# Kernel tuning notes

Hardware: AMD Instinct MI355X
Metric: run time of the kernel (lower is better)

Reference implementation:

```python
import jax, jax.numpy as jnp
import numpy as np

N = 100000   # nodes
E = 1250000  # edges
R = 8        # num_relations
D = 64       # in_channels = hidden = out dim (all 64 per RGIN_Net construction)
L = 2        # max_depth
EPS = 1e-5


def setup_inputs() -> dict:
    key = jax.random.key(0)
    ks = jax.random.split(key, 18)
    s = 1.0 / np.sqrt(D)
    inp = {
        'x': jax.random.normal(ks[0], (N, D), dtype=jnp.float32),
        'edge_index': jax.random.randint(ks[1], (2, E), 0, N, dtype=jnp.int64),
        'edge_type': jax.random.randint(ks[2], (E,), 0, R, dtype=jnp.int64),
        # per-relation MLP params, stacked over L layers and R relations
        'W1': jax.random.normal(ks[3], (L, R, D, D), dtype=jnp.float32) * s,
        'b1': jax.random.normal(ks[4], (L, R, D), dtype=jnp.float32) * 0.01,
        'g1': 1.0 + 0.1 * jax.random.normal(ks[5], (L, R, D), dtype=jnp.float32),
        'be1': jax.random.normal(ks[6], (L, R, D), dtype=jnp.float32) * 0.01,
        'W2': jax.random.normal(ks[7], (L, R, D, D), dtype=jnp.float32) * s,
        'b2': jax.random.normal(ks[8], (L, R, D), dtype=jnp.float32) * 0.01,
        # root MLP params per layer
        'rW1': jax.random.normal(ks[9], (L, D, D), dtype=jnp.float32) * s,
        'rb1': jax.random.normal(ks[10], (L, D), dtype=jnp.float32) * 0.01,
        'rg1': 1.0 + 0.1 * jax.random.normal(ks[11], (L, D), dtype=jnp.float32),
        'rbe1': jax.random.normal(ks[12], (L, D), dtype=jnp.float32) * 0.01,
        'rW2': jax.random.normal(ks[13], (L, D, D), dtype=jnp.float32) * s,
        'rb2': jax.random.normal(ks[14], (L, D), dtype=jnp.float32) * 0.01,
        'bias': jax.random.normal(ks[15], (L, D), dtype=jnp.float32) * 0.01,
    }
    return inp


def _bn(z, gamma, beta, axis):
    # BatchNorm1d in training mode: batch stats, biased variance
    mean = jnp.mean(z, axis=axis, keepdims=True)
    var = jnp.mean(jnp.square(z - mean), axis=axis, keepdims=True)
    return (z - mean) * jax.lax.rsqrt(var + EPS) * gamma + beta


def _forward(x, edge_index, edge_type, W1, b1, g1, be1, W2, b2,
             rW1, rb1, rg1, rbe1, rW2, rb2, bias):
    src, dst = edge_index[0], edge_index[1]
    # combined segment id encodes (relation, dst-node) -> one fused scatter-add
    seg = edge_type * N + dst
    for i in range(L):
        # gather -> scatter-add per relation: h[r, n] = sum_{e: type=r, dst=n} x[src[e]]
        h = jax.ops.segment_sum(x[src], seg, num_segments=R * N).reshape(R, N, D)
        # per-relation MLP: Linear -> BN -> ReLU -> Linear (summed over relations)
        z = jnp.einsum('rnd,rdh->rnh', h, W1[i]) + b1[i][:, None, :]
        z = jax.nn.relu(_bn(z, g1[i][:, None, :], be1[i][:, None, :], axis=1))
        rel = jnp.einsum('rnh,rho->rno', z, W2[i]) + b2[i][:, None, :]
        out = rel.sum(axis=0)
        # root MLP on x itself
        zr = x @ rW1[i] + rb1[i]
        zr = jax.nn.relu(_bn(zr, rg1[i], rbe1[i], axis=0))
        out = out + zr @ rW2[i] + rb2[i] + bias[i]
        x = jax.nn.relu(out) if i + 1 < L else out  # dropout p=0.0
    return x


def reference(x, edge_index, edge_type, W1, b1, g1, be1, W2, b2,
              rW1, rb1, rg1, rbe1, rW2, rb2, bias):
    return _forward(x, edge_index, edge_type, W1, b1, g1, be1, W2, b2,
                    rW1, rb1, rg1, rbe1, rW2, rb2, bias)
```

## Files before the change

### kernel.cpp

```cpp
#include <hip/hip_runtime.h>

#define NN 100000
#define NE 1250000
#define NR 8
#define DD 64
#define TILE 128
#define NTILES 782
#define NBUCKETS (NR * NTILES)
#define CAP 512
#define HROW 72
#define EPSB 1e-5f

typedef unsigned short u16;
typedef unsigned int u32;
typedef __attribute__((ext_vector_type(8))) short short8;
typedef __attribute__((ext_vector_type(4))) float f32x4;

static __device__ __forceinline__ float b2f_lo(u32 v) { return __uint_as_float(v << 16); }
static __device__ __forceinline__ float b2f_hi(u32 v) { return __uint_as_float(v & 0xffff0000u); }
static __device__ __forceinline__ u16 f2b(float f) {
    u32 u = __float_as_uint(f);
    u += 0x7fffu + ((u >> 16) & 1u);
    return (u16)(u >> 16);
}
static __device__ __forceinline__ u32 pk(float a, float b) {
    return (u32)f2b(a) | ((u32)f2b(b) << 16);
}
static __device__ __forceinline__ void acc8(float* acc, uint4 v0, uint4 v1, uint4 v2, uint4 v3) {
#pragma unroll
    for (int q = 0; q < 4; q++) {
        uint4 v = (q == 0) ? v0 : (q == 1) ? v1 : (q == 2) ? v2 : v3;
        acc[q * 8 + 0] += b2f_lo(v.x);
        acc[q * 8 + 1] += b2f_hi(v.x);
        acc[q * 8 + 2] += b2f_lo(v.y);
        acc[q * 8 + 3] += b2f_hi(v.y);
        acc[q * 8 + 4] += b2f_lo(v.z);
        acc[q * 8 + 5] += b2f_hi(v.z);
        acc[q * 8 + 6] += b2f_lo(v.w);
        acc[q * 8 + 7] += b2f_hi(v.w);
    }
}


__global__ void cvt_kernel(const float* __restrict__ in, u16* __restrict__ outb) {
    int i = blockIdx.x * 256 + threadIdx.x;
    if (i < NN * DD / 8) {
        float4 a = *(const float4*)&in[i * 8];
        float4 b = *(const float4*)&in[i * 8 + 4];
        uint4 o;
        o.x = pk(a.x, a.y); o.y = pk(a.z, a.w);
        o.z = pk(b.x, b.y); o.w = pk(b.z, b.w);
        *(uint4*)&outb[i * 8] = o;
    }
}


__global__ void wt_kernel(const float* __restrict__ W1, const float* __restrict__ rW1,
                          const float* __restrict__ W2, const float* __restrict__ rW2,
                          u16* __restrict__ wt1g, u16* __restrict__ wt2g) {
    int m = blockIdx.x;
    int i = m / 18, rest = m % 18;
    int set = rest / 9, r = rest % 9;
    const float* W = (set == 0)
        ? ((r < NR) ? (W1 + ((size_t)i * NR + r) * DD * DD) : (rW1 + (size_t)i * DD * DD))
        : ((r < NR) ? (W2 + ((size_t)i * NR + r) * DD * DD) : (rW2 + (size_t)i * DD * DD));
    u32* dst = (u32*)((set == 0 ? wt1g : wt2g) + ((size_t)i * 9 + r) * DD * DD);
    for (int j = threadIdx.x; j < DD * 32; j += 256) {
        int d = j >> 5, kp = j & 31;
        dst[j] = pk(W[(2 * kp) * DD + d], W[(2 * kp + 1) * DD + d]);
    }
}


__global__ void count_kernel(const int* __restrict__ dst,
                             const int* __restrict__ et,
                             int* __restrict__ cnt) {
    int i = blockIdx.x * 256 + threadIdx.x;
    if (i < NE) atomicAdd(&cnt[et[i] * NTILES + (dst[i] >> 7)], 1);
}

__global__ void scan_kernel(const int* __restrict__ cnt, int* __restrict__ off, int n) {
    __shared__ int ts[1024];
    int t = threadIdx.x;
    int v[8];
    int s = 0;
#pragma unroll
    for (int j = 0; j < 8; j++) {
        int idx = t * 8 + j;
        int c = (idx < n) ? cnt[idx] : 0;
        v[j] = s;
        s += c;
    }
    ts[t] = s;
    __syncthreads();
    for (int d = 1; d < 1024; d <<= 1) {
        int add = (t >= d) ? ts[t - d] : 0;
        __syncthreads();
        ts[t] += add;
        __syncthreads();
    }
    int base = (t > 0) ? ts[t - 1] : 0;
#pragma unroll
    for (int j = 0; j < 8; j++) {
        int idx = t * 8 + j;
        if (idx < n) off[idx] = base + v[j];
    }
    if (t == 1023) off[n] = ts[1023];
}

__global__ void fill_kernel(const int* __restrict__ src, const int* __restrict__ dst,
                            const int* __restrict__ et, const int* __restrict__ off,
                            int* __restrict__ cursor, int* __restrict__ ep) {
    int i = blockIdx.x * 256 + threadIdx.x;
    if (i < NE) {
        int d = dst[i];
        int b = et[i] * NTILES + (d >> 7);
        int pos = off[b] + atomicAdd(&cursor[b], 1);
        ep[pos] = (src[i] << 8) | (d & 127);
    }
}


__launch_bounds__(256, 4)
__global__ void gemm1_kernel(const u16* __restrict__ xb,
                             const int* __restrict__ ep, const int* __restrict__ off,
                             const u16* __restrict__ wt1, const float* __restrict__ b1l,
                             const float* __restrict__ rb1l,
                             u16* __restrict__ zb, float* __restrict__ stats) {
    __shared__ u16 hsb[TILE * HROW];
    __shared__ int seS[CAP], seD[CAP];
    __shared__ int shist[TILE], scur[TILE], soff[TILE + 1];
    __shared__ float red[2 * DD];
    int r = blockIdx.y;
    bool root = (r == NR);
    int n0 = blockIdx.x * TILE;
    int tid = threadIdx.x;

    int wv = tid >> 6;
    int l  = tid & 63;
    int lr = l & 15;
    int lg = l >> 4;

    const u16* wtg = wt1 + (size_t)r * DD * DD;
    short8 bfrg[2][4];
#pragma unroll
    for (int ks = 0; ks < 2; ks++)
#pragma unroll
        for (int ct = 0; ct < 4; ct++)
            bfrg[ks][ct] = *(const short8*)&wtg[(ct * 16 + lr) * DD + ks * 32 + lg * 8];

    if (tid < 128) red[tid] = 0.f;

    if (!root) {
        int b = r * NTILES + blockIdx.x;
        int e0 = off[b], e1 = off[b + 1];
        int m = e1 - e0;
        int slot = tid & 127, half = tid >> 7;
        float acc[32];
#pragma unroll
        for (int j = 0; j < 32; j++) acc[j] = 0.f;

        for (int base = 0; base < m; base += CAP) {
            int cnt = min(m - base, CAP);
            if (tid < TILE) shist[tid] = 0;
            __syncthreads();
            for (int i = tid; i < cnt; i += 256) {
                int p = ep[e0 + base + i];
                seS[i] = p;
                atomicAdd(&shist[p & 127], 1);
            }
            __syncthreads();
            if (tid < TILE) soff[tid + 1] = shist[tid];
            if (tid == 0) soff[0] = 0;
            __syncthreads();
            for (int d = 1; d < TILE; d <<= 1) {
                int v = 0;
                if (tid < TILE && tid >= d) v = soff[tid + 1 - d];
                __syncthreads();
                if (tid < TILE && tid >= d) soff[tid + 1] += v;
                __syncthreads();
            }
            if (tid < TILE) scur[tid] = soff[tid];
            __syncthreads();
            for (int i = tid; i < cnt; i += 256) {
                int p = seS[i];
                seD[atomicAdd(&scur[p & 127], 1)] = p;
            }
            __syncthreads();
            int sb = soff[slot], se = soff[slot + 1];
            int e = sb;
            for (; e + 2 <= se; e += 2) {
                const u16* xr0 = &xb[(size_t)(seD[e] >> 8) * DD + half * 32];
                const u16* xr1 = &xb[(size_t)(seD[e + 1] >> 8) * DD + half * 32];
                uint4 a0 = *(const uint4*)(xr0);      uint4 c0 = *(const uint4*)(xr1);
                uint4 a1 = *(const uint4*)(xr0 + 8);  uint4 c1 = *(const uint4*)(xr1 + 8);
                uint4 a2 = *(const uint4*)(xr0 + 16); uint4 c2 = *(const uint4*)(xr1 + 16);
                uint4 a3 = *(const uint4*)(xr0 + 24); uint4 c3 = *(const uint4*)(xr1 + 24);
                acc8(acc, a0, a1, a2, a3);
                acc8(acc, c0, c1, c2, c3);
            }
            if (e < se) {
                const u16* xr = &xb[(size_t)(seD[e] >> 8) * DD + half * 32];
                acc8(acc, *(const uint4*)(xr), *(const uint4*)(xr + 8),
                     *(const uint4*)(xr + 16), *(const uint4*)(xr + 24));
            }
            __syncthreads();
        }
        u32 pw[16];
#pragma unroll
        for (int j = 0; j < 16; j++) pw[j] = pk(acc[2 * j], acc[2 * j + 1]);
        u16* hrow = &hsb[slot * HROW + half * 32];
        *(uint4*)(hrow)      = make_uint4(pw[0], pw[1], pw[2], pw[3]);
        *(uint4*)(hrow + 8)  = make_uint4(pw[4], pw[5], pw[6], pw[7]);
        *(uint4*)(hrow + 16) = make_uint4(pw[8], pw[9], pw[10], pw[11]);
        *(uint4*)(hrow + 24) = make_uint4(pw[12], pw[13], pw[14], pw[15]);
    } else {
        for (int idx = tid; idx < TILE * 8; idx += 256) {
            int row = idx >> 3, q = idx & 7;
            int n = n0 + row;
            uint4 v = make_uint4(0, 0, 0, 0);
            if (n < NN) v = *(const uint4*)&xb[(size_t)n * DD + q * 8];
            *(uint4*)&hsb[row * HROW + q * 8] = v;
        }
    }
    __syncthreads();

    f32x4 dacc[2][4];
#pragma unroll
    for (int rt = 0; rt < 2; rt++)
#pragma unroll
        for (int ct = 0; ct < 4; ct++) dacc[rt][ct] = (f32x4){0.f, 0.f, 0.f, 0.f};

#pragma unroll
    for (int ks = 0; ks < 2; ks++) {
        short8 afr[2];
#pragma unroll
        for (int rt = 0; rt < 2; rt++)
            afr[rt] = *(const short8*)&hsb[(wv * 32 + rt * 16 + lr) * HROW + ks * 32 + lg * 8];
#pragma unroll
        for (int ct = 0; ct < 4; ct++) {
            dacc[0][ct] = __builtin_amdgcn_mfma_f32_16x16x32_bf16(afr[0], bfrg[ks][ct], dacc[0][ct], 0, 0, 0);
            dacc[1][ct] = __builtin_amdgcn_mfma_f32_16x16x32_bf16(afr[1], bfrg[ks][ct], dacc[1][ct], 0, 0, 0);
        }
    }

    const float* bvec = root ? rb1l : (b1l + r * DD);
    float bv4[4], s1v[4], s2v[4];
#pragma unroll
    for (int ct = 0; ct < 4; ct++) { bv4[ct] = bvec[16 * ct + lr]; s1v[ct] = 0.f; s2v[ct] = 0.f; }
#pragma unroll
    for (int rt = 0; rt < 2; rt++)
#pragma unroll
        for (int ct = 0; ct < 4; ct++)
#pragma unroll
            for (int i = 0; i < 4; i++) {
                float v = dacc[rt][ct][i] + bv4[ct];
                dacc[rt][ct][i] = v;
                int n = n0 + wv * 32 + rt * 16 + lg * 4 + i;
                if (n < NN) { s1v[ct] += v; s2v[ct] += v * v; }
            }
#pragma unroll
    for (int ct = 0; ct < 4; ct++) {
        float a = s1v[ct], bq = s2v[ct];
        a += __shfl_xor(a, 16); bq += __shfl_xor(bq, 16);
        a += __shfl_xor(a, 32); bq += __shfl_xor(bq, 32);
        if (lg == 0) {
            atomicAdd(&red[16 * ct + lr], a);
            atomicAdd(&red[64 + 16 * ct + lr], bq);
        }
    }
    __syncthreads();

#pragma unroll
    for (int rt = 0; rt < 2; rt++)
#pragma unroll
        for (int ct = 0; ct < 4; ct++)
#pragma unroll
            for (int i = 0; i < 4; i++)
                hsb[(wv * 32 + rt * 16 + lg * 4 + i) * HROW + 16 * ct + lr] = f2b(dacc[rt][ct][i]);
    __syncthreads();

    u16* zout = zb + (size_t)r * NN * DD;
    for (int idx = tid; idx < TILE * 8; idx += 256) {
        int row = idx >> 3, q = idx & 7;
        int n = n0 + row;
        if (n < NN)
            *(uint4*)&zout[(size_t)n * DD + q * 8] = *(const uint4*)&hsb[row * HROW + q * 8];
    }
    if (tid < 64) {
        atomicAdd(&stats[r * DD + tid], red[tid]);
        atomicAdd(&stats[576 + r * DD + tid], red[64 + tid]);
    }
}


__global__ void finalize_kernel(const float* __restrict__ stats,
                                const float* __restrict__ g1l, const float* __restrict__ be1l,
                                const float* __restrict__ rg1l, const float* __restrict__ rbe1l,
                                const float* __restrict__ b2l, const float* __restrict__ rb2l,
                                const float* __restrict__ biasl,
                                float* __restrict__ affine, float* __restrict__ constd) {
    int t = threadIdx.x;
    if (t < 576) {
        int r = t >> 6, d = t & 63;
        float mean = stats[t] * (1.f / NN);
        float var = fmaxf(stats[576 + t] * (1.f / NN) - mean * mean, 0.f);
        float g  = (r < NR) ? g1l[r * DD + d]  : rg1l[d];
        float be = (r < NR) ? be1l[r * DD + d] : rbe1l[d];
        float sc = g * rsqrtf(var + EPSB);
        affine[t] = sc;
        affine[576 + t] = be - mean * sc;
        if (r == 0) {
            float cd = rb2l[d] + biasl[d];
#pragma unroll
            for (int rr = 0; rr < NR; rr++) cd += b2l[rr * DD + d];
            constd[d] = cd;
        }
    }
}


__launch_bounds__(256, 4)
__global__ void pass2_kernel(const u16* __restrict__ zb, const u16* __restrict__ wt2,
                             const float* __restrict__ affine, const float* __restrict__ constd,
                             float* __restrict__ outf, u16* __restrict__ outb,
                             int emit_bf16_relu) {
    __shared__ u16 zsb[TILE * HROW];
    __shared__ u16 wtb[DD * HROW];
    int n0 = blockIdx.x * TILE;
    int tid = threadIdx.x;
    int srow = tid >> 3;
    int sc0 = (tid & 7) * 8;

    int wv = tid >> 6;
    int l  = tid & 63;
    int lr = l & 15;
    int lg = l >> 4;

    f32x4 dacc[2][4];
#pragma unroll
    for (int rt = 0; rt < 2; rt++)
#pragma unroll
        for (int ct = 0; ct < 4; ct++) dacc[rt][ct] = (f32x4){0.f, 0.f, 0.f, 0.f};

    uint4 preA[4], preB[4];
#pragma unroll
    for (int q = 0; q < 4; q++) {
        int n = n0 + srow + 32 * q;
        preA[q] = (n < NN) ? *(const uint4*)&zb[(size_t)n * DD + sc0] : make_uint4(0, 0, 0, 0);
        preB[q] = (n < NN) ? *(const uint4*)&zb[(size_t)NN * DD + (size_t)n * DD + sc0]
                           : make_uint4(0, 0, 0, 0);
    }

#pragma unroll
    for (int r = 0; r < 9; r++) {
        uint4* cur = (r & 1) ? preB : preA;
        float4 aLo = *(const float4*)&affine[r * DD + sc0];
        float4 aHi = *(const float4*)&affine[r * DD + sc0 + 4];
        float4 cLo = *(const float4*)&affine[576 + r * DD + sc0];
        float4 cHi = *(const float4*)&affine[576 + r * DD + sc0 + 4];
        __syncthreads();
#pragma unroll
        for (int q = 0; q < 4; q++) {
            uint4 vv = cur[q];
            float a0 = fmaxf(fmaf(b2f_lo(vv.x), aLo.x, cLo.x), 0.f);
            float a1 = fmaxf(fmaf(b2f_hi(vv.x), aLo.y, cLo.y), 0.f);
            float a2 = fmaxf(fmaf(b2f_lo(vv.y), aLo.z, cLo.z), 0.f);
            float a3 = fmaxf(fmaf(b2f_hi(vv.y), aLo.w, cLo.w), 0.f);
            float a4 = fmaxf(fmaf(b2f_lo(vv.z), aHi.x, cHi.x), 0.f);
            float a5 = fmaxf(fmaf(b2f_hi(vv.z), aHi.y, cHi.y), 0.f);
            float a6 = fmaxf(fmaf(b2f_lo(vv.w), aHi.z, cHi.z), 0.f);
            float a7 = fmaxf(fmaf(b2f_hi(vv.w), aHi.w, cHi.w), 0.f);
            uint4 o = make_uint4(pk(a0, a1), pk(a2, a3), pk(a4, a5), pk(a6, a7));
            *(uint4*)&zsb[(srow + 32 * q) * HROW + sc0] = o;
        }
        {
            const u32* wsrc = (const u32*)(wt2 + (size_t)r * DD * DD);
            for (int i2 = tid; i2 < DD * 32; i2 += 256) {
                int row = i2 >> 5, q = i2 & 31;
                ((u32*)&wtb[row * HROW])[q] = wsrc[i2];
            }
        }
        __syncthreads();
        if (r + 2 < 9) {
            const u16* zp = zb + (size_t)(r + 2) * NN * DD;
#pragma unroll
            for (int q = 0; q < 4; q++) {
                int n = n0 + srow + 32 * q;
                cur[q] = (n < NN) ? *(const uint4*)&zp[(size_t)n * DD + sc0]
                                  : make_uint4(0, 0, 0, 0);
            }
        }
#pragma unroll
        for (int ks = 0; ks < 2; ks++) {
            short8 afr[2];
#pragma unroll
            for (int rt = 0; rt < 2; rt++)
                afr[rt] = *(const short8*)&zsb[(wv * 32 + rt * 16 + lr) * HROW + ks * 32 + lg * 8];
#pragma unroll
            for (int ct = 0; ct < 4; ct++) {
                short8 bfr = *(const short8*)&wtb[(ct * 16 + lr) * HROW + ks * 32 + lg * 8];
                dacc[0][ct] = __builtin_amdgcn_mfma_f32_16x16x32_bf16(afr[0], bfr, dacc[0][ct], 0, 0, 0);
                dacc[1][ct] = __builtin_amdgcn_mfma_f32_16x16x32_bf16(afr[1], bfr, dacc[1][ct], 0, 0, 0);
            }
        }
    }

    float cd4[4];
#pragma unroll
    for (int ct = 0; ct < 4; ct++) cd4[ct] = constd[16 * ct + lr];

    if (emit_bf16_relu) {
        __syncthreads();
#pragma unroll
        for (int rt = 0; rt < 2; rt++)
#pragma unroll
            for (int ct = 0; ct < 4; ct++)
#pragma unroll
                for (int i = 0; i < 4; i++) {
                    float v = fmaxf(dacc[rt][ct][i] + cd4[ct], 0.f);
                    zsb[(wv * 32 + rt * 16 + lg * 4 + i) * HROW + 16 * ct + lr] = f2b(v);
                }
        __syncthreads();
        for (int idx = tid; idx < TILE * 8; idx += 256) {
            int row = idx >> 3, q = idx & 7;
            int n = n0 + row;
            if (n < NN)
                *(uint4*)&outb[(size_t)n * DD + q * 8] = *(const uint4*)&zsb[row * HROW + q * 8];
        }
    } else {
        float* zf = (float*)zsb;
#pragma unroll
        for (int h = 0; h < 2; h++) {
            __syncthreads();
#pragma unroll
            for (int rt = 0; rt < 2; rt++)
#pragma unroll
                for (int cc = 0; cc < 2; cc++) {
                    int ct = 2 * h + cc;
#pragma unroll
                    for (int i = 0; i < 4; i++)
                        zf[(wv * 32 + rt * 16 + lg * 4 + i) * 34 + 16 * cc + lr] =
                            dacc[rt][ct][i] + cd4[ct];
                }
            __syncthreads();
            for (int idx = tid; idx < TILE * 8; idx += 256) {
                int row = idx >> 3, q = idx & 7;
                int n = n0 + row;
                if (n < NN)
                    *(float4*)&outf[(size_t)n * DD + 32 * h + q * 4] =
                        *(const float4*)&zf[row * 34 + q * 4];
            }
        }
    }
}


extern "C" void kernel_launch(void* const* d_in, const int* in_sizes, int n_in,
                              void* d_out, int out_size, void* d_ws, size_t ws_size,
                              hipStream_t stream) {
    (void)in_sizes; (void)n_in; (void)out_size;

    const float* x0   = (const float*)d_in[0];
    const int*   ei   = (const int*)d_in[1];
    const int*   et   = (const int*)d_in[2];
    const float* W1   = (const float*)d_in[3];
    const float* b1   = (const float*)d_in[4];
    const float* g1   = (const float*)d_in[5];
    const float* be1  = (const float*)d_in[6];
    const float* W2   = (const float*)d_in[7];
    const float* b2   = (const float*)d_in[8];
    const float* rW1  = (const float*)d_in[9];
    const float* rb1  = (const float*)d_in[10];
    const float* rg1  = (const float*)d_in[11];
    const float* rbe1 = (const float*)d_in[12];
    const float* rW2  = (const float*)d_in[13];
    const float* rb2  = (const float*)d_in[14];
    const float* bias = (const float*)d_in[15];
    float* out = (float*)d_out;

    char* ws = (char*)d_ws;
    size_t zelems = (size_t)9 * NN * DD;
    u16* zb   = (u16*)ws;
    u16* xb   = zb + zelems;
    u16* wt1g = xb + (size_t)NN * DD;
    u16* wt2g = wt1g + 18 * DD * DD;
    float* stats  = (float*)(wt2g + 18 * DD * DD);
    float* affine = stats + 1152;
    float* constd = affine + 1152;
    int* cnt    = (int*)(constd + 64);
    int* cursor = cnt + NBUCKETS;
    int* off    = cursor + NBUCKETS;
    int* ep     = off + NBUCKETS + 1;

    size_t need = (zelems + (size_t)NN * DD + 36 * DD * DD) * 2
                + (1152 + 1152 + 64) * 4
                + ((size_t)3 * NBUCKETS + 1 + NE) * 4;
    if (ws_size < need) return;

    cvt_kernel<<<(NN * DD / 8 + 255) / 256, 256, 0, stream>>>(x0, xb);
    wt_kernel<<<36, 256, 0, stream>>>(W1, rW1, W2, rW2, wt1g, wt2g);
    hipMemsetAsync(cnt, 0, sizeof(int) * 2 * NBUCKETS, stream);
    count_kernel<<<(NE + 255) / 256, 256, 0, stream>>>(ei + NE, et, cnt);
    scan_kernel<<<1, 1024, 0, stream>>>(cnt, off, NBUCKETS);
    fill_kernel<<<(NE + 255) / 256, 256, 0, stream>>>(ei, ei + NE, et, off, cursor, ep);

    for (int i = 0; i < 2; i++) {
        hipMemsetAsync(stats, 0, sizeof(float) * 1152, stream);
        gemm1_kernel<<<dim3(NTILES, 9), 256, 0, stream>>>(
            xb, ep, off,
            wt1g + (size_t)i * 9 * DD * DD,
            b1 + (size_t)i * NR * DD, rb1 + (size_t)i * DD,
            zb, stats);
        finalize_kernel<<<1, 576, 0, stream>>>(
            stats,
            g1 + (size_t)i * NR * DD, be1 + (size_t)i * NR * DD,
            rg1 + (size_t)i * DD, rbe1 + (size_t)i * DD,
            b2 + (size_t)i * NR * DD, rb2 + (size_t)i * DD, bias + (size_t)i * DD,
            affine, constd);
        pass2_kernel<<<NTILES, 256, 0, stream>>>(
            zb, wt2g + (size_t)i * 9 * DD * DD,
            affine, constd, out, xb, (i == 0) ? 1 : 0);
    }
}
```

Measured before the change: 493.7 us.

## Use wave-shuffle bucket scan, prefetch W2 into registers, raise gemm1 occupancy

In gemm1, the barrier-heavy shared-memory prefix scan over the 128 per-tile histogram bins becomes a single-wave shuffle scan, and the trailing barrier of the chunk loop is dropped. The weight-fragment load moves after the gather phase so its registers are not live during accumulation, and launch bounds go from 4 to 6 blocks per CU. In gemm2, the next relation's W2 tile is prefetched into registers during the current MFMA phase rather than loaded synchronously into LDS. Raising the occupancy target risks register spills in the gather loop.

Measured after the change: 500.8 us. About the same (+1.4%).

```diff
diff --git a/kernel.cpp b/kernel.cpp
--- a/kernel.cpp
+++ b/kernel.cpp
@@ -121,7 +121,7 @@
 }
 
 
-__launch_bounds__(256, 4)
+__launch_bounds__(256, 6)
 __global__ void gemm1_kernel(const u16* __restrict__ xb,
                              const int* __restrict__ ep, const int* __restrict__ off,
                              const u16* __restrict__ wt1, const float* __restrict__ b1l,
@@ -129,7 +129,8 @@
                              u16* __restrict__ zb, float* __restrict__ stats) {
     __shared__ u16 hsb[TILE * HROW];
     __shared__ int seS[CAP], seD[CAP];
-    __shared__ int shist[TILE], scur[TILE], soff[TILE + 1];
+    __shared__ int shist[TILE], scur[TILE];
+    __shared__ int soff[TILE + 1];
     __shared__ float red[2 * DD];
     int r = blockIdx.y;
     bool root = (r == NR);
@@ -140,14 +141,6 @@
     int l  = tid & 63;
     int lr = l & 15;
     int lg = l >> 4;
-
-    const u16* wtg = wt1 + (size_t)r * DD * DD;
-    short8 bfrg[2][4];
-#pragma unroll
-    for (int ks = 0; ks < 2; ks++)
-#pragma unroll
-        for (int ct = 0; ct < 4; ct++)
-            bfrg[ks][ct] = *(const short8*)&wtg[(ct * 16 + lr) * DD + ks * 32 + lg * 8];
 
     if (tid < 128) red[tid] = 0.f;
 
@@ -170,17 +163,22 @@
                 atomicAdd(&shist[p & 127], 1);
             }
             __syncthreads();
-            if (tid < TILE) soff[tid + 1] = shist[tid];
-            if (tid == 0) soff[0] = 0;
-            __syncthreads();
-            for (int d = 1; d < TILE; d <<= 1) {
-                int v = 0;
-                if (tid < TILE && tid >= d) v = soff[tid + 1 - d];
-                __syncthreads();
-                if (tid < TILE && tid >= d) soff[tid + 1] += v;
-                __syncthreads();
-            }
-            if (tid < TILE) scur[tid] = soff[tid];
+            if (tid < 64) {
+                int c0 = shist[tid], c1 = shist[tid + 64];
+                int s0 = c0, s1 = c1;
+#pragma unroll
+                for (int d = 1; d < 64; d <<= 1) {
+                    int t0 = __shfl_up(s0, d);
+                    int t1 = __shfl_up(s1, d);
+                    if (tid >= d) { s0 += t0; s1 += t1; }
+                }
+                int tot0 = __shfl(s0, 63);
+                soff[tid + 1]  = s0;
+                soff[tid + 65] = tot0 + s1;
+                if (tid == 0) soff[0] = 0;
+                scur[tid]      = s0 - c0;
+                scur[tid + 64] = tot0 + s1 - c1;
+            }
             __syncthreads();
             for (int i = tid; i < cnt; i += 256) {
                 int p = seS[i];
@@ -204,7 +202,6 @@
                 acc8(acc, *(const uint4*)(xr), *(const uint4*)(xr + 8),
                      *(const uint4*)(xr + 16), *(const uint4*)(xr + 24));
             }
-            __syncthreads();
         }
         u32 pw[16];
 #pragma unroll
@@ -223,6 +220,14 @@
             *(uint4*)&hsb[row * HROW + q * 8] = v;
         }
     }
+
+    const u16* wtg = wt1 + (size_t)r * DD * DD;
+    short8 bfrg[2][4];
+#pragma unroll
+    for (int ks = 0; ks < 2; ks++)
+#pragma unroll
+        for (int ct = 0; ct < 4; ct++)
+            bfrg[ks][ct] = *(const short8*)&wtg[(ct * 16 + lr) * DD + ks * 32 + lg * 8];
     __syncthreads();
 
     f32x4 dacc[2][4];
@@ -344,12 +349,18 @@
         for (int ct = 0; ct < 4; ct++) dacc[rt][ct] = (f32x4){0.f, 0.f, 0.f, 0.f};
 
     uint4 preA[4], preB[4];
+    u32 wreg[8];
 #pragma unroll
     for (int q = 0; q < 4; q++) {
         int n = n0 + srow + 32 * q;
         preA[q] = (n < NN) ? *(const uint4*)&zb[(size_t)n * DD + sc0] : make_uint4(0, 0, 0, 0);
         preB[q] = (n < NN) ? *(const uint4*)&zb[(size_t)NN * DD + (size_t)n * DD + sc0]
                            : make_uint4(0, 0, 0, 0);
+    }
+    {
+        const u32* wsrc = (const u32*)wt2;
+#pragma unroll
+        for (int j = 0; j < 8; j++) wreg[j] = wsrc[tid + 256 * j];
     }
 
 #pragma unroll
@@ -375,13 +386,17 @@
             *(uint4*)&zsb[(srow + 32 * q) * HROW + sc0] = o;
         }
         {
-            const u32* wsrc = (const u32*)(wt2 + (size_t)r * DD * DD);
-            for (int i2 = tid; i2 < DD * 32; i2 += 256) {
-                int row = i2 >> 5, q = i2 & 31;
-                ((u32*)&wtb[row * HROW])[q] = wsrc[i2];
-            }
+            int row = tid >> 5, q = tid & 31;
+#pragma unroll
+            for (int j = 0; j < 8; j++)
+                ((u32*)&wtb[(row + 8 * j) * HROW])[q] = wreg[j];
         }
         __syncthreads();
+        if (r + 1 < 9) {
+            const u32* wsrc = (const u32*)(wt2 + (size_t)(r + 1) * DD * DD);
+#pragma unroll
+            for (int j = 0; j < 8; j++) wreg[j] = wsrc[tid + 256 * j];
+        }
         if (r + 2 < 9) {
             const u16* zp = zb + (size_t)(r + 2) * NN * DD;
 #pragma unroll
```
